# Kernel tuning notes

Measured on AMD Instinct MI355X. Metric: run time of the kernel, lower is better.

Reference implementation:

```python
import jax, jax.numpy as jnp
import numpy as np

OUT_F, IN_F = 4096, 4096
GROUP = 128
NGROUPS = IN_F // GROUP  # 32


def setup_inputs() -> dict:
    key = jax.random.key(0)
    k1, k2, k3, k4 = jax.random.split(key, 4)
    x = jax.random.normal(k1, (4, 2048, IN_F), dtype=jnp.float32)
    # 4-bit codes stored as integers in [0, 16)
    compressed_weight = jax.random.randint(k2, (OUT_F, IN_F), 0, 16, dtype=jnp.int32)
    scale = jax.random.uniform(k3, (OUT_F, NGROUPS), dtype=jnp.float32)
    offset = jax.random.normal(k4, (OUT_F, NGROUPS), dtype=jnp.float32)
    return {"x": x, "compressed_weight": compressed_weight, "scale": scale, "offset": offset}


def reference(x, compressed_weight, scale, offset):
    # group-wise dequant: w[o, g, j] = code * scale[o, g] - offset[o, g]
    codes = compressed_weight.astype(scale.dtype).reshape(OUT_F, NGROUPS, GROUP)
    w = (codes * scale[..., None] - offset[..., None]).reshape(OUT_F, IN_F)
    # F.linear: x @ w.T  -> [B, S, OUT_F]
    return jnp.einsum('bsi,oi->bso', x, w.astype(x.dtype))
```

## Files before the change

kernel.cpp:

```cpp
#include <hip/hip_runtime.h>
#include <stdint.h>

#define OUT_F 4096
#define IN_F  4096
#define NGROUPS 32
#define BK 64
#define NT (IN_F / BK)

typedef __attribute__((ext_vector_type(4)))  float    f32x4;
typedef __attribute__((ext_vector_type(16))) float    f32x16;
typedef __attribute__((ext_vector_type(8)))  short    bf16x8;
typedef __attribute__((ext_vector_type(4)))  int      i32x4;
typedef __attribute__((ext_vector_type(4)))  uint32_t u32x4;

__device__ __forceinline__ ushort f2bf(float f) {
  union { float f; uint32_t u; } v; v.f = f;
  uint32_t r = v.u + 0x7FFFu + ((v.u >> 16) & 1u);
  return (ushort)(r >> 16);
}

__global__ void cvt_x_kernel(const float* __restrict__ x, ushort* __restrict__ xb, int n8) {
  int i = blockIdx.x * blockDim.x + threadIdx.x;
  if (i >= n8) return;
  const f32x4* xp = (const f32x4*)x;
  f32x4 a = xp[2 * i], b = xp[2 * i + 1];
  u32x4 o;
  o.x = (uint32_t)f2bf(a.x) | ((uint32_t)f2bf(a.y) << 16);
  o.y = (uint32_t)f2bf(a.z) | ((uint32_t)f2bf(a.w) << 16);
  o.z = (uint32_t)f2bf(b.x) | ((uint32_t)f2bf(b.y) << 16);
  o.w = (uint32_t)f2bf(b.z) | ((uint32_t)f2bf(b.w) << 16);
  ((u32x4*)xb)[i] = o;
}

__global__ void dequant_w_kernel(const int* __restrict__ cw,
                                 const float* __restrict__ sc,
                                 const float* __restrict__ of,
                                 ushort* __restrict__ wb) {
  int t = blockIdx.x * blockDim.x + threadIdx.x;
  int o  = t >> 9;
  int k0 = (t & 511) << 3;
  int g  = k0 >> 7;
  float s   = sc[o * NGROUPS + g];
  float off = of[o * NGROUPS + g];
  const i32x4* cp = (const i32x4*)(cw + (size_t)o * IN_F + k0);
  i32x4 c0 = cp[0], c1 = cp[1];
  u32x4 out;
  out.x = (uint32_t)f2bf((float)c0.x * s - off) | ((uint32_t)f2bf((float)c0.y * s - off) << 16);
  out.y = (uint32_t)f2bf((float)c0.z * s - off) | ((uint32_t)f2bf((float)c0.w * s - off) << 16);
  out.z = (uint32_t)f2bf((float)c1.x * s - off) | ((uint32_t)f2bf((float)c1.y * s - off) << 16);
  out.w = (uint32_t)f2bf((float)c1.z * s - off) | ((uint32_t)f2bf((float)c1.w * s - off) << 16);
  *(u32x4*)(wb + (size_t)o * IN_F + k0) = out;
}


#define BAR() do { asm volatile("" ::: "memory"); __builtin_amdgcn_s_barrier(); asm volatile("" ::: "memory"); } while (0)

#define GLLDS(gp, lp) __builtin_amdgcn_global_load_lds( \
  (const __attribute__((address_space(1))) uint32_t*)(const void*)(gp), \
  (__attribute__((address_space(3))) uint32_t*)(void*)(lp), 16, 0, 0)

#define STAGE_A(buf, kt) do { \
  _Pragma("unroll") for (int q_ = 0; q_ < 4; ++q_) \
    GLLDS(A + (size_t)(m0 + q_ * 64 + stRow) * IN_F + (kt) * BK + sl * 8, \
          ldsb + (buf) * 65536 + q_ * 8192 + wid * 1024); \
} while (0)

#define STAGE_B(buf, kt) do { \
  _Pragma("unroll") for (int q_ = 0; q_ < 4; ++q_) \
    GLLDS(B + (size_t)(n0 + q_ * 64 + stRow) * IN_F + (kt) * BK + sl * 8, \
          ldsb + (buf) * 65536 + 32768 + q_ * 8192 + wid * 1024); \
} while (0)

#define RD_SLICE(SET, S, aX, bX) do { \
  _Pragma("unroll") for (int i_ = 0; i_ < 4; ++i_) \
    A_[SET][i_] = *(const bf16x8*)((aX) + (i_ * 32 + lw) * 128 + kOff[S]); \
  _Pragma("unroll") for (int j_ = 0; j_ < 2; ++j_) \
    B_[SET][j_] = *(const bf16x8*)((bX) + (j_ * 32 + lw) * 128 + kOff[S]); \
} while (0)

#define MFMA_SLICE(SET) do { \
  __builtin_amdgcn_s_setprio(1); \
  _Pragma("unroll") for (int i_ = 0; i_ < 4; ++i_) \
  _Pragma("unroll") for (int j_ = 0; j_ < 2; ++j_) \
    acc[i_][j_] = __builtin_amdgcn_mfma_f32_32x32x16_bf16(A_[SET][i_], B_[SET][j_], acc[i_][j_], 0, 0, 0); \
  __builtin_amdgcn_s_setprio(0); \
} while (0)

__global__ __launch_bounds__(512, 2) void gemm256(const ushort* __restrict__ A,
                                                  const ushort* __restrict__ B,
                                                  float* __restrict__ C, int M) {
  __shared__ ushort lds[65536];
  char* ldsb = (char*)lds;

  const int nmt = M >> 8;
  const int nwg = gridDim.x;
  int wg = blockIdx.x;
  if ((nwg & 7) == 0) wg = (wg & 7) * (nwg >> 3) + (wg >> 3);
  const int bn = wg / nmt;
  const int bm = wg % nmt;
  const int m0 = bm << 8, n0 = bn << 8;

  const int tid  = threadIdx.x;
  const int lane = tid & 63;
  const int wid  = tid >> 6;
  const int wr   = wid >> 2;
  const int wc   = wid & 3;

  const int stRow = wid * 8 + (lane >> 3);
  const int sl    = (lane & 7) ^ (lane >> 3);

  const int lw = lane & 31;
  const int h  = lane >> 5;
  int kOff[4];
#pragma unroll
  for (int s = 0; s < 4; ++s) kOff[s] = ((2 * s + h) ^ (lane & 7)) << 4;

  f32x16 acc[4][2] = {};
  bf16x8 A_[2][4], B_[2][2];

  STAGE_A(0, 0); STAGE_B(0, 0);
  STAGE_A(1, 1); STAGE_B(1, 1);
  asm volatile("s_waitcnt vmcnt(8)" ::: "memory");
  BAR();
  RD_SLICE(0, 0, ldsb + wr * 16384, ldsb + 32768 + wc * 8192);

#pragma unroll 1
  for (int t = 0; t < NT; ++t) {
    const int cur = t & 1, nxt = cur ^ 1;
    const char* aC = ldsb + cur * 65536 + wr * 16384;
    const char* bC = ldsb + cur * 65536 + 32768 + wc * 8192;
    const char* aN = ldsb + nxt * 65536 + wr * 16384;
    const char* bN = ldsb + nxt * 65536 + 32768 + wc * 8192;

    RD_SLICE(1, 1, aC, bC);
    MFMA_SLICE(0);
    RD_SLICE(0, 2, aC, bC);
    MFMA_SLICE(1);
    BAR();

    RD_SLICE(1, 3, aC, bC);
    if (t + 2 < NT) { STAGE_A(cur, t + 2); STAGE_B(cur, t + 2); }
    MFMA_SLICE(0);
    if (t + 2 < NT)      { asm volatile("s_waitcnt vmcnt(8)" ::: "memory"); }
    else if (t + 1 < NT) { asm volatile("s_waitcnt vmcnt(0)" ::: "memory"); }
    BAR();
    if (t + 1 < NT) RD_SLICE(0, 0, aN, bN);
    MFMA_SLICE(1);
  }

  const int crow = m0 + wr * 128;
  const int ccol = n0 + wc * 64 + lw;
#pragma unroll
  for (int i = 0; i < 4; ++i)
#pragma unroll
    for (int j = 0; j < 2; ++j)
#pragma unroll
      for (int p = 0; p < 4; ++p)
#pragma unroll
        for (int q = 0; q < 4; ++q)
          C[(size_t)(crow + i * 32 + 8 * p + 4 * h + q) * OUT_F + (ccol + j * 32)] = acc[i][j][4 * p + q];
}

__global__ void naive_kernel(const float* __restrict__ x, const int* __restrict__ cw,
                             const float* __restrict__ sc, const float* __restrict__ of,
                             float* __restrict__ out, int M) {
  int idx = blockIdx.x * blockDim.x + threadIdx.x;
  if (idx >= M * OUT_F) return;
  int o = idx & (OUT_F - 1);
  int m = idx >> 12;
  const float* xr = x + (size_t)m * IN_F;
  const int*   wr = cw + (size_t)o * IN_F;
  float acc = 0.f;
  for (int gg = 0; gg < NGROUPS; ++gg) {
    float s = sc[o * NGROUPS + gg], off = of[o * NGROUPS + gg];
#pragma unroll 8
    for (int k = 0; k < 128; ++k) {
      int kk = (gg << 7) + k;
      acc += xr[kk] * ((float)wr[kk] * s - off);
    }
  }
  out[idx] = acc;
}

extern "C" void kernel_launch(void* const* d_in, const int* in_sizes, int n_in,
                              void* d_out, int out_size, void* d_ws, size_t ws_size,
                              hipStream_t stream) {
  const float* x  = (const float*)d_in[0];
  const int*   cw = (const int*)d_in[1];
  const float* sc = (const float*)d_in[2];
  const float* of = (const float*)d_in[3];
  float* out = (float*)d_out;
  const int M = in_sizes[0] / IN_F;

  const size_t xb_bytes = (size_t)M * IN_F * 2;
  const size_t wb_bytes = (size_t)OUT_F * IN_F * 2;

  if (ws_size >= xb_bytes + wb_bytes && (M % 256) == 0) {
    ushort* xb = (ushort*)d_ws;
    ushort* wb = (ushort*)((char*)d_ws + xb_bytes);

    int n8 = (M * IN_F) / 8;
    cvt_x_kernel<<<(n8 + 255) / 256, 256, 0, stream>>>(x, xb, n8);

    int nw8 = (OUT_F * IN_F) / 8;
    dequant_w_kernel<<<(nw8 + 255) / 256, 256, 0, stream>>>(cw, sc, of, wb);

    dim3 grid((M / 256) * (OUT_F / 256));
    gemm256<<<grid, 512, 0, stream>>>(xb, wb, out, M);
  } else {
    int total = M * OUT_F;
    naive_kernel<<<(total + 255) / 256, 256, 0, stream>>>(x, cw, sc, of, out, M);
  }
}
```

Before: 313.6 us.

## Switch GEMM to 16x16x32 MFMA with quadrant-split LDS reads and staggered staging

Replaces the 32x32x16 bf16 MFMA tiling with 16x16x32 MFMAs over an 8x4 accumulator grid, reading A and B fragments in half-tiles and interleaving them with MFMA quadrants. The A and B global-to-LDS staging for tile t+2 is split across two barrier phases with adjusted vmcnt waits. It also adds an explicit lgkmcnt(0) wait before the first barrier. The aim is finer-grained overlap of LDS reads with MFMA work. The cost is more MFMA instructions and a more complex synchronisation schedule that could add stalls.

```diff
diff --git a/kernel.cpp b/kernel.cpp
--- a/kernel.cpp
+++ b/kernel.cpp
@@ -8,7 +8,6 @@
 #define NT (IN_F / BK)
 
 typedef __attribute__((ext_vector_type(4)))  float    f32x4;
-typedef __attribute__((ext_vector_type(16))) float    f32x16;
 typedef __attribute__((ext_vector_type(8)))  short    bf16x8;
 typedef __attribute__((ext_vector_type(4)))  int      i32x4;
 typedef __attribute__((ext_vector_type(4)))  uint32_t u32x4;
@@ -71,18 +70,21 @@
           ldsb + (buf) * 65536 + 32768 + q_ * 8192 + wid * 1024); \
 } while (0)
 
-#define RD_SLICE(SET, S, aX, bX) do { \
+#define RD_AH(dst, i0, base, H, OFF) do { \
   _Pragma("unroll") for (int i_ = 0; i_ < 4; ++i_) \
-    A_[SET][i_] = *(const bf16x8*)((aX) + (i_ * 32 + lw) * 128 + kOff[S]); \
+    dst[i_][H] = *(const bf16x8*)((base) + ((i0) + i_) * 2048 + (OFF)); \
+} while (0)
+
+#define RD_BH(dst, j0, base, H, OFF) do { \
   _Pragma("unroll") for (int j_ = 0; j_ < 2; ++j_) \
-    B_[SET][j_] = *(const bf16x8*)((bX) + (j_ * 32 + lw) * 128 + kOff[S]); \
-} while (0)
-
-#define MFMA_SLICE(SET) do { \
+    dst[j_][H] = *(const bf16x8*)((base) + ((j0) + j_) * 2048 + (OFF)); \
+} while (0)
+
+#define MFMAH(I0, J0, Aset, Bset, H) do { \
   __builtin_amdgcn_s_setprio(1); \
   _Pragma("unroll") for (int i_ = 0; i_ < 4; ++i_) \
   _Pragma("unroll") for (int j_ = 0; j_ < 2; ++j_) \
-    acc[i_][j_] = __builtin_amdgcn_mfma_f32_32x32x16_bf16(A_[SET][i_], B_[SET][j_], acc[i_][j_], 0, 0, 0); \
+    acc[(I0) + i_][(J0) + j_] = __builtin_amdgcn_mfma_f32_16x16x32_bf16(Aset[i_][H], Bset[j_][H], acc[(I0) + i_][(J0) + j_], 0, 0, 0); \
   __builtin_amdgcn_s_setprio(0); \
 } while (0)
 
@@ -109,20 +111,20 @@
   const int stRow = wid * 8 + (lane >> 3);
   const int sl    = (lane & 7) ^ (lane >> 3);
 
-  const int lw = lane & 31;
-  const int h  = lane >> 5;
-  int kOff[4];
-#pragma unroll
-  for (int s = 0; s < 4; ++s) kOff[s] = ((2 * s + h) ^ (lane & 7)) << 4;
-
-  f32x16 acc[4][2] = {};
-  bf16x8 A_[2][4], B_[2][2];
+  const int frow = lane & 15;
+  const int g    = lane >> 4;
+  const int off0 = frow * 128 + (((g    ) ^ (lane & 7)) << 4);
+  const int off1 = frow * 128 + (((4 + g) ^ (lane & 7)) << 4);
+
+  f32x4 acc[8][4] = {};
+  bf16x8 A0_[4][2], A1_[4][2], B0_[2][2], B1_[2][2];
 
   STAGE_A(0, 0); STAGE_B(0, 0);
   STAGE_A(1, 1); STAGE_B(1, 1);
   asm volatile("s_waitcnt vmcnt(8)" ::: "memory");
   BAR();
-  RD_SLICE(0, 0, ldsb + wr * 16384, ldsb + 32768 + wc * 8192);
+  RD_AH(A0_, 0, ldsb + wr * 16384, 0, off0);
+  RD_BH(B0_, 0, ldsb + 32768 + wc * 8192, 0, off0);
 
 #pragma unroll 1
   for (int t = 0; t < NT; ++t) {
@@ -132,33 +134,48 @@
     const char* aN = ldsb + nxt * 65536 + wr * 16384;
     const char* bN = ldsb + nxt * 65536 + 32768 + wc * 8192;
 
-    RD_SLICE(1, 1, aC, bC);
-    MFMA_SLICE(0);
-    RD_SLICE(0, 2, aC, bC);
-    MFMA_SLICE(1);
+    RD_BH(B1_, 2, bC, 0, off0);
+    RD_AH(A1_, 4, aC, 0, off0);
+    MFMAH(0, 0, A0_, B0_, 0);
+
+    RD_AH(A0_, 0, aC, 1, off1);
+    MFMAH(0, 2, A0_, B1_, 0);
+
+    RD_BH(B0_, 0, bC, 1, off1);
+    MFMAH(4, 0, A1_, B0_, 0);
+
+    RD_BH(B1_, 2, bC, 1, off1);
+    RD_AH(A1_, 4, aC, 1, off1);
+    MFMAH(4, 2, A1_, B1_, 0);
+
+    MFMAH(0, 0, A0_, B0_, 1);
+    asm volatile("s_waitcnt lgkmcnt(0)" ::: "memory");
+    if (t + 1 < NT) { asm volatile("s_waitcnt vmcnt(4)" ::: "memory"); }
     BAR();
 
-    RD_SLICE(1, 3, aC, bC);
-    if (t + 2 < NT) { STAGE_A(cur, t + 2); STAGE_B(cur, t + 2); }
-    MFMA_SLICE(0);
-    if (t + 2 < NT)      { asm volatile("s_waitcnt vmcnt(8)" ::: "memory"); }
+    if (t + 1 < NT) RD_AH(A0_, 0, aN, 0, off0);
+    if (t + 2 < NT) STAGE_A(cur, t + 2);
+    MFMAH(0, 2, A0_, B1_, 1);
+    if (t + 2 < NT)      { asm volatile("s_waitcnt vmcnt(4)" ::: "memory"); }
     else if (t + 1 < NT) { asm volatile("s_waitcnt vmcnt(0)" ::: "memory"); }
     BAR();
-    if (t + 1 < NT) RD_SLICE(0, 0, aN, bN);
-    MFMA_SLICE(1);
+
+    if (t + 1 < NT) RD_BH(B0_, 0, bN, 0, off0);
+    if (t + 2 < NT) STAGE_B(cur, t + 2);
+    MFMAH(4, 0, A1_, B0_, 1);
+
+    MFMAH(4, 2, A1_, B1_, 1);
   }
 
-  const int crow = m0 + wr * 128;
-  const int ccol = n0 + wc * 64 + lw;
+  const int crow0 = m0 + wr * 128 + (g << 2);
+  const int ccol0 = n0 + wc * 64 + frow;
 #pragma unroll
-  for (int i = 0; i < 4; ++i)
+  for (int mf = 0; mf < 8; ++mf)
 #pragma unroll
-    for (int j = 0; j < 2; ++j)
+    for (int nf = 0; nf < 4; ++nf)
 #pragma unroll
-      for (int p = 0; p < 4; ++p)
-#pragma unroll
-        for (int q = 0; q < 4; ++q)
-          C[(size_t)(crow + i * 32 + 8 * p + 4 * h + q) * OUT_F + (ccol + j * 32)] = acc[i][j][4 * p + q];
+      for (int q = 0; q < 4; ++q)
+        C[(size_t)(crow0 + mf * 16 + q) * OUT_F + (ccol0 + nf * 16)] = acc[mf][nf][q];
 }
 
 __global__ void naive_kernel(const float* __restrict__ x, const int* __restrict__ cw,
```

After: 286.8 us. -8.6%, faster.
